# Optimization experiments

Hardware: AMD Instinct MI355X
Metric: run time of the kernel (lower is better)

## Reference

```python
import jax, jax.numpy as jnp
import numpy as np

N = 50000        # nodes
E = 1250000      # edges
B = 512          # graphs
DIN, DH, DOUT = 64, 64, 16


def setup_inputs() -> dict:
    key = jax.random.key(0)
    ks = jax.random.split(key, 8)
    s = lambda d: np.float32(1.0 / np.sqrt(d))
    return {
        "x": jax.random.normal(ks[0], (N, DIN), jnp.float32),
        "edge_index": jax.random.randint(ks[1], (2, E), 0, N, dtype=jnp.int32),
        "batch": jnp.sort(jax.random.randint(ks[2], (N,), 0, B, dtype=jnp.int32)),
        "W1": jax.random.normal(ks[3], (DH, DIN), jnp.float32) * s(DIN),
        "b1": jnp.zeros((DH,), jnp.float32),
        "W2": jax.random.normal(ks[4], (DH, DH), jnp.float32) * s(DH),
        "b2": jnp.zeros((DH,), jnp.float32),
        "W3": jax.random.normal(ks[5], (DH, DH), jnp.float32) * s(DH),
        "b3": jnp.zeros((DH,), jnp.float32),
        "Wl": jax.random.normal(ks[6], (DOUT, DH), jnp.float32) * s(DH),
        "bl": jnp.zeros((DOUT,), jnp.float32),
    }


def _gcn_conv(x, src, dst, norm, W, b, n):
    # PyG GCNConv: h = x W^T; out[i] = sum_{(j->i)} norm_ji * h[j] + b
    h = x @ W.T                                   # [N, DH]
    msg = h[src] * norm[:, None]                  # [E+N, DH] gather
    return jax.ops.segment_sum(msg, dst, num_segments=n) + b


def reference(x, edge_index, batch, W1, b1, W2, b2, W3, b3, Wl, bl):
    n = x.shape[0]
    loop = jnp.arange(n, dtype=edge_index.dtype)
    # add self-loops (PyG GCNConv default add_self_loops=True)
    src = jnp.concatenate([edge_index[0], loop])
    dst = jnp.concatenate([edge_index[1], loop])
    # symmetric normalization: deg^{-1/2}[src] * deg^{-1/2}[dst]
    deg = jax.ops.segment_sum(jnp.ones_like(src, jnp.float32), dst, num_segments=n)
    dinv = jax.lax.rsqrt(deg)                     # deg >= 1 thanks to self-loops
    norm = dinv[src] * dinv[dst]

    h = x
    for W, b in ((W1, b1), (W2, b2), (W3, b3)):
        h = jax.nn.relu(_gcn_conv(h, src, dst, norm, W, b, n))

    # global mean pool over each graph
    sums = jax.ops.segment_sum(h, batch, num_segments=B)          # [B, DH]
    cnts = jax.ops.segment_sum(jnp.ones((n,), jnp.float32), batch, num_segments=B)
    pooled = sums / jnp.maximum(cnts, 1.0)[:, None]
    # dropout p=0.5 is identity in eval mode
    return pooled @ Wl.T + bl                                     # [B, DOUT]
```

## Files before the change

kernel.cpp:

```cpp
#include <hip/hip_runtime.h>
#include <hip/hip_fp16.h>


#define CAPB 3072
#define BINTILE 4096

__global__ __launch_bounds__(256) void init_kernel(int* __restrict__ fctr) {
    int idx = blockIdx.x * blockDim.x + threadIdx.x;
    if (idx < 512) fctr[idx] = 0;
}

__global__ __launch_bounds__(256) void bin512_kernel(const int* __restrict__ src,
                                                     const int* __restrict__ dst,
                                                     int* __restrict__ fctr,
                                                     int2* __restrict__ recs2,
                                                     int e, int n) {
    __shared__ int lcnt[512], gbase[512];
    int tid = threadIdx.x;
    int s0  = blockIdx.x * BINTILE;
    lcnt[tid] = 0;
    lcnt[tid + 256] = 0;
    __syncthreads();
    int dv[16], bk[16];
#pragma unroll
    for (int k = 0; k < 16; ++k) {
        int i = s0 + tid + k * 256;
        if (i < e) {
            dv[k] = dst[i];
            bk[k] = (int)((512LL * dv[k]) / n);
            atomicAdd(&lcnt[bk[k]], 1);
        } else {
            bk[k] = -1;
        }
    }
    __syncthreads();
#pragma unroll
    for (int j = 0; j < 2; ++j) {
        int b = tid + j * 256;
        gbase[b] = b * CAPB + atomicAdd(&fctr[b], lcnt[b]);
        lcnt[b]  = 0;
    }
    __syncthreads();
#pragma unroll
    for (int k = 0; k < 16; ++k) {
        if (bk[k] >= 0) {
            int i = s0 + tid + k * 256;
            int p = gbase[bk[k]] + atomicAdd(&lcnt[bk[k]], 1);
            if (p < (bk[k] + 1) * CAPB) recs2[p] = make_int2(src[i], dv[k]);
        }
    }
}

__global__ __launch_bounds__(256) void sortfill_mm_kernel(
    const int2* __restrict__ recs2, const int* __restrict__ fctr,
    int* __restrict__ rp, float* __restrict__ dinv, int* __restrict__ csr,
    const float* __restrict__ x, const float* __restrict__ W1,
    __half* __restrict__ t1, int n) {
    __shared__ int hist[128];
    __shared__ int lofs[129];
    __shared__ int stage[CAPB];
    __shared__ int redbuf[256];
    __shared__ float xrow[98 * 64];
    int g   = blockIdx.x;
    int N0  = (int)(((long long)n * g + 511) / 512);
    int N1  = (int)(((long long)n * (g + 1) + 511) / 512);
    int nn  = N1 - N0;
    int tid = threadIdx.x;
    int lane = tid & 63;
    int wave = tid >> 6;

    int partial = 0;
    for (int j = tid; j < g; j += 256) partial += min(fctr[j], CAPB);
    redbuf[tid] = partial;
    if (tid < 128) hist[tid] = 0;
    __syncthreads();
    for (int s = 128; s > 0; s >>= 1) {
        if (tid < s) redbuf[tid] += redbuf[tid + s];
        __syncthreads();
    }
    int base = redbuf[0];
    const int2* my = recs2 + (size_t)g * CAPB;
    int total = min(fctr[g], CAPB);
    for (int i = tid; i < total; i += 256)
        atomicAdd(&hist[my[i].y - N0], 1);
    __syncthreads();
    if (tid == 0) {
        int acc = 0;
        for (int k = 0; k < nn; ++k) { lofs[k] = acc; acc += hist[k]; }
        lofs[nn] = acc;
    }
    __syncthreads();
    if (tid < 128) hist[tid] = 0;
    __syncthreads();
    for (int i = tid; i < total; i += 256) {
        int2 rec = my[i];
        int  li  = rec.y - N0;
        int  pos = lofs[li] + atomicAdd(&hist[li], 1);
        stage[pos] = rec.x;
    }
    __syncthreads();
    for (int j = tid; j < total; j += 256) csr[base + j] = stage[j];
    if (tid < nn) {
        rp[N0 + tid]   = base + lofs[tid];
        int deg        = lofs[tid + 1] - lofs[tid];
        dinv[N0 + tid] = rsqrtf((float)(deg + 1));
    }
    if (g == 511 && tid == 0) rp[n] = base + total;

    for (int idx = tid; idx < nn * 16; idx += 256)
        ((float4*)xrow)[idx] = ((const float4*)(x + (size_t)N0 * 64))[idx];
    float4 wreg[16];
    const float4* W4 = (const float4*)(W1 + lane * 64);
#pragma unroll
    for (int q = 0; q < 16; ++q) wreg[q] = W4[q];
    __syncthreads();
    for (int li = wave; li < nn; li += 4) {
        float dv = rsqrtf((float)(lofs[li + 1] - lofs[li] + 1));
        const float4* row = (const float4*)(xrow + li * 64);
        float acc = 0.0f;
#pragma unroll
        for (int q = 0; q < 16; ++q) {
            float4 hv = row[q];
            acc += hv.x * wreg[q].x + hv.y * wreg[q].y +
                   hv.z * wreg[q].z + hv.w * wreg[q].w;
        }
        t1[(size_t)(N0 + li) * 64 + lane] = __float2half(acc * dv);
    }
}

__global__ __launch_bounds__(256) void mm_kernel(const float* __restrict__ h,
                                                 const float* __restrict__ W,
                                                 const float* __restrict__ dinv,
                                                 __half* __restrict__ t, int n) {
    __shared__ float hs[64 * 64];
    int tid  = threadIdx.x;
    int lane = tid & 63;
    int wave = tid >> 6;
    int base = blockIdx.x * 64;

    float4 wreg[16];
    const float4* W4 = (const float4*)(W + lane * 64);
#pragma unroll
    for (int q = 0; q < 16; ++q) wreg[q] = W4[q];

    int nrows = min(64, n - base);
    const float4* h4  = (const float4*)(h + (size_t)base * 64);
    float4*       hs4 = (float4*)hs;
    for (int idx = tid; idx < nrows * 16; idx += 256) hs4[idx] = h4[idx];
    __syncthreads();

    for (int r = wave * 16; r < wave * 16 + 16; ++r) {
        int i = base + r;
        if (i >= n) break;
        const float4* row = (const float4*)(hs + r * 64);
        float acc = 0.0f;
#pragma unroll
        for (int q = 0; q < 16; ++q) {
            float4 hv = row[q];
            acc += hv.x * wreg[q].x + hv.y * wreg[q].y +
                   hv.z * wreg[q].z + hv.w * wreg[q].w;
        }
        t[(size_t)i * 64 + lane] = __float2half(acc * dinv[i]);
    }
}

__global__ __launch_bounds__(256) void agg_kernel(const __half* __restrict__ t,
                                                  const int* __restrict__ rp,
                                                  const int* __restrict__ cs,
                                                  const float* __restrict__ dinv,
                                                  const float* __restrict__ bias,
                                                  float* __restrict__ hout, int n) {
    int gw   = (blockIdx.x * blockDim.x + threadIdx.x) >> 6;
    int lane = threadIdx.x & 63;
    if (gw >= n) return;
    int i   = gw;
    int grp = lane >> 4;
    int fo  = (lane & 15) << 2;
    int beg = rp[i];
    int end = rp[i + 1];

    float4 a0 = make_float4(0.f, 0.f, 0.f, 0.f);
    float4 a1 = a0, a2 = a0, a3 = a0;
    int e = beg + grp;
    for (; e + 12 < end; e += 16) {
        int s0 = cs[e];
        int s1 = cs[e + 4];
        int s2 = cs[e + 8];
        int s3 = cs[e + 12];
        uint2 u0 = *(const uint2*)(t + (size_t)s0 * 64 + fo);
        uint2 u1 = *(const uint2*)(t + (size_t)s1 * 64 + fo);
        uint2 u2 = *(const uint2*)(t + (size_t)s2 * 64 + fo);
        uint2 u3 = *(const uint2*)(t + (size_t)s3 * 64 + fo);
        float2 f;
        f = __half22float2(*(const __half2*)&u0.x); a0.x += f.x; a0.y += f.y;
        f = __half22float2(*(const __half2*)&u0.y); a0.z += f.x; a0.w += f.y;
        f = __half22float2(*(const __half2*)&u1.x); a1.x += f.x; a1.y += f.y;
        f = __half22float2(*(const __half2*)&u1.y); a1.z += f.x; a1.w += f.y;
        f = __half22float2(*(const __half2*)&u2.x); a2.x += f.x; a2.y += f.y;
        f = __half22float2(*(const __half2*)&u2.y); a2.z += f.x; a2.w += f.y;
        f = __half22float2(*(const __half2*)&u3.x); a3.x += f.x; a3.y += f.y;
        f = __half22float2(*(const __half2*)&u3.y); a3.z += f.x; a3.w += f.y;
    }
    for (; e < end; e += 4) {
        int s = cs[e];
        uint2 u = *(const uint2*)(t + (size_t)s * 64 + fo);
        float2 f;
        f = __half22float2(*(const __half2*)&u.x); a1.x += f.x; a1.y += f.y;
        f = __half22float2(*(const __half2*)&u.y); a1.z += f.x; a1.w += f.y;
    }
    float4 acc;
    acc.x = (a0.x + a1.x) + (a2.x + a3.x);
    acc.y = (a0.y + a1.y) + (a2.y + a3.y);
    acc.z = (a0.z + a1.z) + (a2.z + a3.z);
    acc.w = (a0.w + a1.w) + (a2.w + a3.w);
    acc.x += __shfl_xor(acc.x, 16, 64);
    acc.y += __shfl_xor(acc.y, 16, 64);
    acc.z += __shfl_xor(acc.z, 16, 64);
    acc.w += __shfl_xor(acc.w, 16, 64);
    acc.x += __shfl_xor(acc.x, 32, 64);
    acc.y += __shfl_xor(acc.y, 32, 64);
    acc.z += __shfl_xor(acc.z, 32, 64);
    acc.w += __shfl_xor(acc.w, 32, 64);
    if (grp == 0) {
        uint2 su = *(const uint2*)(t + (size_t)i * 64 + fo);
        float2 s01 = __half22float2(*(const __half2*)&su.x);
        float2 s23 = __half22float2(*(const __half2*)&su.y);
        float4 bv = *(const float4*)(bias + fo);
        float  dv = dinv[i];
        float4 o;
        o.x = fmaxf(fmaf(dv, acc.x + s01.x, bv.x), 0.0f);
        o.y = fmaxf(fmaf(dv, acc.y + s01.y, bv.y), 0.0f);
        o.z = fmaxf(fmaf(dv, acc.z + s23.x, bv.z), 0.0f);
        o.w = fmaxf(fmaf(dv, acc.w + s23.y, bv.w), 0.0f);
        *(float4*)(hout + (size_t)i * 64 + fo) = o;
    }
}

__global__ __launch_bounds__(256) void poolfinal_kernel(const float* __restrict__ h,
                                                        const int* __restrict__ batch,
                                                        const float* __restrict__ Wl,
                                                        const float* __restrict__ bl,
                                                        float* __restrict__ out,
                                                        int n) {
    __shared__ float red[4][64];
    int b    = blockIdx.x;
    int tid  = threadIdx.x;
    int lane = tid & 63;
    int w    = tid >> 6;
    int l = 0, r = n;
    while (l < r) { int m = (l + r) >> 1; if (batch[m] < b) l = m + 1; else r = m; }
    int lo = l;
    r = n;
    while (l < r) { int m = (l + r) >> 1; if (batch[m] < b + 1) l = m + 1; else r = m; }
    int hi = l;
    float acc = 0.0f;
    for (int i = lo + w; i < hi; i += 4) acc += h[(size_t)i * 64 + lane];
    red[w][lane] = acc;
    __syncthreads();
    if (w == 0) {
        float s = (red[0][lane] + red[1][lane]) + (red[2][lane] + red[3][lane]);
        float c = (float)(hi - lo);
        red[0][lane] = s / fmaxf(c, 1.0f);
    }
    __syncthreads();
    if (tid < 16) {
        float a = bl[tid];
        const float* wr = Wl + tid * 64;
#pragma unroll
        for (int k = 0; k < 64; ++k) a += red[0][k] * wr[k];
        out[b * 16 + tid] = a;
    }
}

extern "C" void kernel_launch(void* const* d_in, const int* in_sizes, int n_in,
                              void* d_out, int out_size, void* d_ws, size_t ws_size,
                              hipStream_t stream) {
    const float* x    = (const float*)d_in[0];
    const int*   ei   = (const int*)d_in[1];
    const int*   batch= (const int*)d_in[2];
    const float* W1   = (const float*)d_in[3];
    const float* b1   = (const float*)d_in[4];
    const float* W2   = (const float*)d_in[5];
    const float* b2   = (const float*)d_in[6];
    const float* W3   = (const float*)d_in[7];
    const float* b3   = (const float*)d_in[8];
    const float* Wl   = (const float*)d_in[9];
    const float* bl   = (const float*)d_in[10];
    float* out = (float*)d_out;

    int n  = in_sizes[0] / 64;
    int e  = in_sizes[1] / 2;
    int nb = out_size / 16;

    const int* esrc = ei;
    const int* edst = ei + e;

    char* p = (char*)d_ws;
    auto carve = [&](size_t bytes) {
        char* r = p;
        p += (bytes + 255) & ~(size_t)255;
        return r;
    };
    size_t featBytes = (size_t)n * 64 * 4;
    size_t recsBytes = (size_t)512 * CAPB * 8;
    size_t bufBBytes = recsBytes > featBytes ? recsBytes : featBytes;

    float*  dinv = (float*)carve((size_t)n * 4);
    int*    rp   = (int*)  carve((size_t)(n + 1) * 4);
    int*    csr  = (int*)  carve((size_t)e * 4);
    __half* bufT = (__half*)carve((size_t)n * 64 * 2);
    float*  bufB = (float*)carve(bufBBytes);
    int*    fctr = (int*)  carve(512 * 4);
    int2*   recs2 = (int2*)bufB;

    dim3 blk(256);
    int gBIN = (e + BINTILE - 1) / BINTILE;
    int gMM  = (n + 63) / 64;
    int gAGG = (n + 3) / 4;

    init_kernel<<<2, blk, 0, stream>>>(fctr);
    bin512_kernel<<<gBIN, blk, 0, stream>>>(esrc, edst, fctr, recs2, e, n);
    sortfill_mm_kernel<<<512, blk, 0, stream>>>(recs2, fctr, rp, dinv, csr,
                                                x, W1, bufT, n);
    agg_kernel<<<gAGG, blk, 0, stream>>>(bufT, rp, csr, dinv, b1, bufB, n);
    mm_kernel<<<gMM, blk, 0, stream>>>(bufB, W2, dinv, bufT, n);
    agg_kernel<<<gAGG, blk, 0, stream>>>(bufT, rp, csr, dinv, b2, bufB, n);
    mm_kernel<<<gMM, blk, 0, stream>>>(bufB, W3, dinv, bufT, n);
    agg_kernel<<<gAGG, blk, 0, stream>>>(bufT, rp, csr, dinv, b3, bufB, n);
    poolfinal_kernel<<<nb, blk, 0, stream>>>(bufB, batch, Wl, bl, out, n);
}
```

Measured before the change: 308.8 us.

## Fuse GCN aggregation with next-layer matmul and final pooling/linear

Each aggregation kernel now also applies the following layer's weight matrix directly in registers using readlane broadcasts, writing fp16 features for the next layer. This removes the separate mm kernels and the fp32 intermediate feature round trip. The last aggregation projects each node through Wl and atomically adds the count-scaled result into the output, replacing the pooling kernel. Per-graph inverse counts and bias initialisation move into the init kernel. The cost is more per-wave ALU and readlane work, contended atomics on 512x16 outputs, and a float summation order that varies between runs.

```diff
diff --git a/kernel.cpp b/kernel.cpp
--- a/kernel.cpp
+++ b/kernel.cpp
@@ -5,9 +5,28 @@
 #define CAPB 3072
 #define BINTILE 4096
 
-__global__ __launch_bounds__(256) void init_kernel(int* __restrict__ fctr) {
-    int idx = blockIdx.x * blockDim.x + threadIdx.x;
-    if (idx < 512) fctr[idx] = 0;
+__device__ __forceinline__ float rl_f(float v, int l) {
+    return __int_as_float(__builtin_amdgcn_readlane(__float_as_int(v), l));
+}
+
+__global__ __launch_bounds__(256) void init_kernel(int* __restrict__ fctr,
+                                                   const int* __restrict__ batch,
+                                                   const float* __restrict__ bl,
+                                                   float* __restrict__ invc,
+                                                   float* __restrict__ out,
+                                                   int n, int nb) {
+    int t = blockIdx.x * blockDim.x + threadIdx.x;
+    if (t < 512) fctr[t] = 0;
+    if (t < nb) {
+        int l = 0, r = n;
+        while (l < r) { int m = (l + r) >> 1; if (batch[m] < t) l = m + 1; else r = m; }
+        int lo = l;
+        r = n;
+        while (l < r) { int m = (l + r) >> 1; if (batch[m] < t + 1) l = m + 1; else r = m; }
+        invc[t] = 1.0f / fmaxf((float)(l - lo), 1.0f);
+#pragma unroll
+        for (int o = 0; o < 16; ++o) out[t * 16 + o] = bl[o];
+    }
 }
 
 __global__ __launch_bounds__(256) void bin512_kernel(const int* __restrict__ src,
@@ -128,48 +147,13 @@
     }
 }
 
-__global__ __launch_bounds__(256) void mm_kernel(const float* __restrict__ h,
-                                                 const float* __restrict__ W,
-                                                 const float* __restrict__ dinv,
-                                                 __half* __restrict__ t, int n) {
-    __shared__ float hs[64 * 64];
-    int tid  = threadIdx.x;
-    int lane = tid & 63;
-    int wave = tid >> 6;
-    int base = blockIdx.x * 64;
-
-    float4 wreg[16];
-    const float4* W4 = (const float4*)(W + lane * 64);
-#pragma unroll
-    for (int q = 0; q < 16; ++q) wreg[q] = W4[q];
-
-    int nrows = min(64, n - base);
-    const float4* h4  = (const float4*)(h + (size_t)base * 64);
-    float4*       hs4 = (float4*)hs;
-    for (int idx = tid; idx < nrows * 16; idx += 256) hs4[idx] = h4[idx];
-    __syncthreads();
-
-    for (int r = wave * 16; r < wave * 16 + 16; ++r) {
-        int i = base + r;
-        if (i >= n) break;
-        const float4* row = (const float4*)(hs + r * 64);
-        float acc = 0.0f;
-#pragma unroll
-        for (int q = 0; q < 16; ++q) {
-            float4 hv = row[q];
-            acc += hv.x * wreg[q].x + hv.y * wreg[q].y +
-                   hv.z * wreg[q].z + hv.w * wreg[q].w;
-        }
-        t[(size_t)i * 64 + lane] = __float2half(acc * dinv[i]);
-    }
-}
-
-__global__ __launch_bounds__(256) void agg_kernel(const __half* __restrict__ t,
-                                                  const int* __restrict__ rp,
-                                                  const int* __restrict__ cs,
-                                                  const float* __restrict__ dinv,
-                                                  const float* __restrict__ bias,
-                                                  float* __restrict__ hout, int n) {
+__global__ __launch_bounds__(256) void aggmm_kernel(const __half* __restrict__ t,
+                                                    const int* __restrict__ rp,
+                                                    const int* __restrict__ cs,
+                                                    const float* __restrict__ dinv,
+                                                    const float* __restrict__ bias,
+                                                    const float* __restrict__ W,
+                                                    __half* __restrict__ tout, int n) {
     int gw   = (blockIdx.x * blockDim.x + threadIdx.x) >> 6;
     int lane = threadIdx.x & 63;
     if (gw >= n) return;
@@ -221,54 +205,143 @@
     acc.y += __shfl_xor(acc.y, 32, 64);
     acc.z += __shfl_xor(acc.z, 32, 64);
     acc.w += __shfl_xor(acc.w, 32, 64);
-    if (grp == 0) {
-        uint2 su = *(const uint2*)(t + (size_t)i * 64 + fo);
-        float2 s01 = __half22float2(*(const __half2*)&su.x);
-        float2 s23 = __half22float2(*(const __half2*)&su.y);
-        float4 bv = *(const float4*)(bias + fo);
-        float  dv = dinv[i];
-        float4 o;
-        o.x = fmaxf(fmaf(dv, acc.x + s01.x, bv.x), 0.0f);
-        o.y = fmaxf(fmaf(dv, acc.y + s01.y, bv.y), 0.0f);
-        o.z = fmaxf(fmaf(dv, acc.z + s23.x, bv.z), 0.0f);
-        o.w = fmaxf(fmaf(dv, acc.w + s23.y, bv.w), 0.0f);
-        *(float4*)(hout + (size_t)i * 64 + fo) = o;
-    }
-}
-
-__global__ __launch_bounds__(256) void poolfinal_kernel(const float* __restrict__ h,
-                                                        const int* __restrict__ batch,
-                                                        const float* __restrict__ Wl,
-                                                        const float* __restrict__ bl,
-                                                        float* __restrict__ out,
-                                                        int n) {
-    __shared__ float red[4][64];
-    int b    = blockIdx.x;
-    int tid  = threadIdx.x;
-    int lane = tid & 63;
-    int w    = tid >> 6;
-    int l = 0, r = n;
-    while (l < r) { int m = (l + r) >> 1; if (batch[m] < b) l = m + 1; else r = m; }
-    int lo = l;
-    r = n;
-    while (l < r) { int m = (l + r) >> 1; if (batch[m] < b + 1) l = m + 1; else r = m; }
-    int hi = l;
-    float acc = 0.0f;
-    for (int i = lo + w; i < hi; i += 4) acc += h[(size_t)i * 64 + lane];
-    red[w][lane] = acc;
-    __syncthreads();
-    if (w == 0) {
-        float s = (red[0][lane] + red[1][lane]) + (red[2][lane] + red[3][lane]);
-        float c = (float)(hi - lo);
-        red[0][lane] = s / fmaxf(c, 1.0f);
-    }
-    __syncthreads();
-    if (tid < 16) {
-        float a = bl[tid];
-        const float* wr = Wl + tid * 64;
-#pragma unroll
-        for (int k = 0; k < 64; ++k) a += red[0][k] * wr[k];
-        out[b * 16 + tid] = a;
+
+    uint2 su = *(const uint2*)(t + (size_t)i * 64 + fo);
+    float2 s01 = __half22float2(*(const __half2*)&su.x);
+    float2 s23 = __half22float2(*(const __half2*)&su.y);
+    float4 bv = *(const float4*)(bias + fo);
+    float  dv = dinv[i];
+    float4 h4;
+    h4.x = fmaxf(fmaf(dv, acc.x + s01.x, bv.x), 0.0f);
+    h4.y = fmaxf(fmaf(dv, acc.y + s01.y, bv.y), 0.0f);
+    h4.z = fmaxf(fmaf(dv, acc.z + s23.x, bv.z), 0.0f);
+    h4.w = fmaxf(fmaf(dv, acc.w + s23.y, bv.w), 0.0f);
+
+    const float4* W4 = (const float4*)(W + lane * 64);
+    float om = 0.0f;
+    __builtin_amdgcn_sched_barrier(0);
+    {
+        float4 wreg[8];
+#pragma unroll
+        for (int q = 0; q < 8; ++q) wreg[q] = W4[q];
+#pragma unroll
+        for (int c = 0; c < 8; ++c) {
+            om = fmaf(rl_f(h4.x, c), wreg[c].x, om);
+            om = fmaf(rl_f(h4.y, c), wreg[c].y, om);
+            om = fmaf(rl_f(h4.z, c), wreg[c].z, om);
+            om = fmaf(rl_f(h4.w, c), wreg[c].w, om);
+        }
+    }
+    __builtin_amdgcn_sched_barrier(0);
+    {
+        float4 wreg[8];
+#pragma unroll
+        for (int q = 0; q < 8; ++q) wreg[q] = W4[8 + q];
+#pragma unroll
+        for (int c = 0; c < 8; ++c) {
+            om = fmaf(rl_f(h4.x, c + 8), wreg[c].x, om);
+            om = fmaf(rl_f(h4.y, c + 8), wreg[c].y, om);
+            om = fmaf(rl_f(h4.z, c + 8), wreg[c].z, om);
+            om = fmaf(rl_f(h4.w, c + 8), wreg[c].w, om);
+        }
+    }
+    tout[(size_t)i * 64 + lane] = __float2half(om * dv);
+}
+
+__global__ __launch_bounds__(256) void aggfinal_kernel(const __half* __restrict__ t,
+                                                       const int* __restrict__ rp,
+                                                       const int* __restrict__ cs,
+                                                       const float* __restrict__ dinv,
+                                                       const float* __restrict__ bias,
+                                                       const float* __restrict__ Wl,
+                                                       const int* __restrict__ batch,
+                                                       const float* __restrict__ invc,
+                                                       float* __restrict__ out, int n) {
+    int gw   = (blockIdx.x * blockDim.x + threadIdx.x) >> 6;
+    int lane = threadIdx.x & 63;
+    if (gw >= n) return;
+    int i   = gw;
+    int grp = lane >> 4;
+    int fo  = (lane & 15) << 2;
+    int beg = rp[i];
+    int end = rp[i + 1];
+
+    float4 a0 = make_float4(0.f, 0.f, 0.f, 0.f);
+    float4 a1 = a0, a2 = a0, a3 = a0;
+    int e = beg + grp;
+    for (; e + 12 < end; e += 16) {
+        int s0 = cs[e];
+        int s1 = cs[e + 4];
+        int s2 = cs[e + 8];
+        int s3 = cs[e + 12];
+        uint2 u0 = *(const uint2*)(t + (size_t)s0 * 64 + fo);
+        uint2 u1 = *(const uint2*)(t + (size_t)s1 * 64 + fo);
+        uint2 u2 = *(const uint2*)(t + (size_t)s2 * 64 + fo);
+        uint2 u3 = *(const uint2*)(t + (size_t)s3 * 64 + fo);
+        float2 f;
+        f = __half22float2(*(const __half2*)&u0.x); a0.x += f.x; a0.y += f.y;
+        f = __half22float2(*(const __half2*)&u0.y); a0.z += f.x; a0.w += f.y;
+        f = __half22float2(*(const __half2*)&u1.x); a1.x += f.x; a1.y += f.y;
+        f = __half22float2(*(const __half2*)&u1.y); a1.z += f.x; a1.w += f.y;
+        f = __half22float2(*(const __half2*)&u2.x); a2.x += f.x; a2.y += f.y;
+        f = __half22float2(*(const __half2*)&u2.y); a2.z += f.x; a2.w += f.y;
+        f = __half22float2(*(const __half2*)&u3.x); a3.x += f.x; a3.y += f.y;
+        f = __half22float2(*(const __half2*)&u3.y); a3.z += f.x; a3.w += f.y;
+    }
+    for (; e < end; e += 4) {
+        int s = cs[e];
+        uint2 u = *(const uint2*)(t + (size_t)s * 64 + fo);
+        float2 f;
+        f = __half22float2(*(const __half2*)&u.x); a1.x += f.x; a1.y += f.y;
+        f = __half22float2(*(const __half2*)&u.y); a1.z += f.x; a1.w += f.y;
+    }
+    float4 acc;
+    acc.x = (a0.x + a1.x) + (a2.x + a3.x);
+    acc.y = (a0.y + a1.y) + (a2.y + a3.y);
+    acc.z = (a0.z + a1.z) + (a2.z + a3.z);
+    acc.w = (a0.w + a1.w) + (a2.w + a3.w);
+    acc.x += __shfl_xor(acc.x, 16, 64);
+    acc.y += __shfl_xor(acc.y, 16, 64);
+    acc.z += __shfl_xor(acc.z, 16, 64);
+    acc.w += __shfl_xor(acc.w, 16, 64);
+    acc.x += __shfl_xor(acc.x, 32, 64);
+    acc.y += __shfl_xor(acc.y, 32, 64);
+    acc.z += __shfl_xor(acc.z, 32, 64);
+    acc.w += __shfl_xor(acc.w, 32, 64);
+
+    uint2 su = *(const uint2*)(t + (size_t)i * 64 + fo);
+    float2 s01 = __half22float2(*(const __half2*)&su.x);
+    float2 s23 = __half22float2(*(const __half2*)&su.y);
+    float4 bv = *(const float4*)(bias + fo);
+    float  dv = dinv[i];
+    float4 h4;
+    h4.x = fmaxf(fmaf(dv, acc.x + s01.x, bv.x), 0.0f);
+    h4.y = fmaxf(fmaf(dv, acc.y + s01.y, bv.y), 0.0f);
+    h4.z = fmaxf(fmaf(dv, acc.z + s23.x, bv.z), 0.0f);
+    h4.w = fmaxf(fmaf(dv, acc.w + s23.y, bv.w), 0.0f);
+
+    __builtin_amdgcn_sched_barrier(0);
+    float4 wl0 = *(const float4*)(Wl + (0 * 4 + grp) * 64 + fo);
+    float4 wl1 = *(const float4*)(Wl + (1 * 4 + grp) * 64 + fo);
+    float4 wl2 = *(const float4*)(Wl + (2 * 4 + grp) * 64 + fo);
+    float4 wl3 = *(const float4*)(Wl + (3 * 4 + grp) * 64 + fo);
+    float z0 = h4.x * wl0.x + h4.y * wl0.y + h4.z * wl0.z + h4.w * wl0.w;
+    float z1 = h4.x * wl1.x + h4.y * wl1.y + h4.z * wl1.z + h4.w * wl1.w;
+    float z2 = h4.x * wl2.x + h4.y * wl2.y + h4.z * wl2.z + h4.w * wl2.w;
+    float z3 = h4.x * wl3.x + h4.y * wl3.y + h4.z * wl3.z + h4.w * wl3.w;
+#pragma unroll
+    for (int s = 1; s <= 8; s <<= 1) {
+        z0 += __shfl_xor(z0, s, 64);
+        z1 += __shfl_xor(z1, s, 64);
+        z2 += __shfl_xor(z2, s, 64);
+        z3 += __shfl_xor(z3, s, 64);
+    }
+    int m = lane & 15;
+    if (m < 4) {
+        int   b  = batch[i];
+        float ic = invc[b];
+        float zv = (m == 0) ? z0 : (m == 1) ? z1 : (m == 2) ? z2 : z3;
+        atomicAdd(out + b * 16 + (m * 4 + grp), zv * ic);
     }
 }
 
@@ -301,31 +374,25 @@
         p += (bytes + 255) & ~(size_t)255;
         return r;
     };
-    size_t featBytes = (size_t)n * 64 * 4;
-    size_t recsBytes = (size_t)512 * CAPB * 8;
-    size_t bufBBytes = recsBytes > featBytes ? recsBytes : featBytes;
-
-    float*  dinv = (float*)carve((size_t)n * 4);
-    int*    rp   = (int*)  carve((size_t)(n + 1) * 4);
-    int*    csr  = (int*)  carve((size_t)e * 4);
-    __half* bufT = (__half*)carve((size_t)n * 64 * 2);
-    float*  bufB = (float*)carve(bufBBytes);
-    int*    fctr = (int*)  carve(512 * 4);
-    int2*   recs2 = (int2*)bufB;
+    float*  dinv  = (float*)carve((size_t)n * 4);
+    int*    rp    = (int*)  carve((size_t)(n + 1) * 4);
+    int*    csr   = (int*)  carve((size_t)e * 4);
+    __half* tA    = (__half*)carve((size_t)n * 64 * 2);
+    __half* tB    = (__half*)carve((size_t)n * 64 * 2);
+    int2*   recs2 = (int2*) carve((size_t)512 * CAPB * 8);
+    int*    fctr  = (int*)  carve(512 * 4);
+    float*  invc  = (float*)carve((size_t)nb * 4);
 
     dim3 blk(256);
     int gBIN = (e + BINTILE - 1) / BINTILE;
-    int gMM  = (n + 63) / 64;
     int gAGG = (n + 3) / 4;
 
-    init_kernel<<<2, blk, 0, stream>>>(fctr);
+    init_kernel<<<2, blk, 0, stream>>>(fctr, batch, bl, invc, out, n, nb);
     bin512_kernel<<<gBIN, blk, 0, stream>>>(esrc, edst, fctr, recs2, e, n);
     sortfill_mm_kernel<<<512, blk, 0, stream>>>(recs2, fctr, rp, dinv, csr,
-                                                x, W1, bufT, n);
-    agg_kernel<<<gAGG, blk, 0, stream>>>(bufT, rp, csr, dinv, b1, bufB, n);
-    mm_kernel<<<gMM, blk, 0, stream>>>(bufB, W2, dinv, bufT, n);
-    agg_kernel<<<gAGG, blk, 0, stream>>>(bufT, rp, csr, dinv, b2, bufB, n);
-    mm_kernel<<<gMM, blk, 0, stream>>>(bufB, W3, dinv, bufT, n);
-    agg_kernel<<<gAGG, blk, 0, stream>>>(bufT, rp, csr, dinv, b3, bufB, n);
-    poolfinal_kernel<<<nb, blk, 0, stream>>>(bufB, batch, Wl, bl, out, n);
-}
+                                                x, W1, tA, n);
+    aggmm_kernel<<<gAGG, blk, 0, stream>>>(tA, rp, csr, dinv, b1, W2, tB, n);
+    aggmm_kernel<<<gAGG, blk, 0, stream>>>(tB, rp, csr, dinv, b2, W3, tA, n);
+    aggfinal_kernel<<<gAGG, blk, 0, stream>>>(tA, rp, csr, dinv, b3, Wl,
+                                              batch, invc, out, n);
+}
```

Result: slower. 400.7 us (+29.8%).

## Fuse final aggregation with mean-pool and linear head via atomics; rebalance edge loops

Applied to the files above, without the earlier changes.

The last aggregation kernel now applies the output linear layer per node, scales by a precomputed inverse graph size, and atomically adds into the output. This removes the final hidden-feature write and the separate pooling kernel. The init kernel precomputes per-graph inverse counts and seeds the output with the bias. The aggregation loop now splits each node's edges into four contiguous chunks, processes them with a masked, 8-way unrolled loop, and adds an occupancy hint to launch bounds. The trade-off is about 200k float atomics into only 8k output slots, which will contend heavily, and a change in summation order.

```diff
diff --git a/kernel.cpp b/kernel.cpp
--- a/kernel.cpp
+++ b/kernel.cpp
@@ -5,9 +5,24 @@
 #define CAPB 3072
 #define BINTILE 4096
 
-__global__ __launch_bounds__(256) void init_kernel(int* __restrict__ fctr) {
-    int idx = blockIdx.x * blockDim.x + threadIdx.x;
-    if (idx < 512) fctr[idx] = 0;
+__global__ __launch_bounds__(256) void init_kernel(int* __restrict__ fctr,
+                                                   const int* __restrict__ batch,
+                                                   const float* __restrict__ bl,
+                                                   float* __restrict__ invc,
+                                                   float* __restrict__ out,
+                                                   int n, int nb) {
+    int t = blockIdx.x * blockDim.x + threadIdx.x;
+    if (t < 512) fctr[t] = 0;
+    if (t < nb) {
+        int l = 0, r = n;
+        while (l < r) { int m = (l + r) >> 1; if (batch[m] < t) l = m + 1; else r = m; }
+        int lo = l;
+        r = n;
+        while (l < r) { int m = (l + r) >> 1; if (batch[m] < t + 1) l = m + 1; else r = m; }
+        invc[t] = 1.0f / fmaxf((float)(l - lo), 1.0f);
+#pragma unroll
+        for (int o = 0; o < 16; ++o) out[t * 16 + o] = bl[o];
+    }
 }
 
 __global__ __launch_bounds__(256) void bin512_kernel(const int* __restrict__ src,
@@ -164,12 +179,12 @@
     }
 }
 
-__global__ __launch_bounds__(256) void agg_kernel(const __half* __restrict__ t,
-                                                  const int* __restrict__ rp,
-                                                  const int* __restrict__ cs,
-                                                  const float* __restrict__ dinv,
-                                                  const float* __restrict__ bias,
-                                                  float* __restrict__ hout, int n) {
+__global__ __launch_bounds__(256, 6) void agg_kernel(const __half* __restrict__ t,
+                                                     const int* __restrict__ rp,
+                                                     const int* __restrict__ cs,
+                                                     const float* __restrict__ dinv,
+                                                     const float* __restrict__ bias,
+                                                     float* __restrict__ hout, int n) {
     int gw   = (blockIdx.x * blockDim.x + threadIdx.x) >> 6;
     int lane = threadIdx.x & 63;
     if (gw >= n) return;
@@ -178,41 +193,39 @@
     int fo  = (lane & 15) << 2;
     int beg = rp[i];
     int end = rp[i + 1];
-
-    float4 a0 = make_float4(0.f, 0.f, 0.f, 0.f);
-    float4 a1 = a0, a2 = a0, a3 = a0;
-    int e = beg + grp;
-    for (; e + 12 < end; e += 16) {
-        int s0 = cs[e];
-        int s1 = cs[e + 4];
-        int s2 = cs[e + 8];
-        int s3 = cs[e + 12];
-        uint2 u0 = *(const uint2*)(t + (size_t)s0 * 64 + fo);
-        uint2 u1 = *(const uint2*)(t + (size_t)s1 * 64 + fo);
-        uint2 u2 = *(const uint2*)(t + (size_t)s2 * 64 + fo);
-        uint2 u3 = *(const uint2*)(t + (size_t)s3 * 64 + fo);
-        float2 f;
-        f = __half22float2(*(const __half2*)&u0.x); a0.x += f.x; a0.y += f.y;
-        f = __half22float2(*(const __half2*)&u0.y); a0.z += f.x; a0.w += f.y;
-        f = __half22float2(*(const __half2*)&u1.x); a1.x += f.x; a1.y += f.y;
-        f = __half22float2(*(const __half2*)&u1.y); a1.z += f.x; a1.w += f.y;
-        f = __half22float2(*(const __half2*)&u2.x); a2.x += f.x; a2.y += f.y;
-        f = __half22float2(*(const __half2*)&u2.y); a2.z += f.x; a2.w += f.y;
-        f = __half22float2(*(const __half2*)&u3.x); a3.x += f.x; a3.y += f.y;
-        f = __half22float2(*(const __half2*)&u3.y); a3.z += f.x; a3.w += f.y;
-    }
-    for (; e < end; e += 4) {
-        int s = cs[e];
-        uint2 u = *(const uint2*)(t + (size_t)s * 64 + fo);
-        float2 f;
-        f = __half22float2(*(const __half2*)&u.x); a1.x += f.x; a1.y += f.y;
-        f = __half22float2(*(const __half2*)&u.y); a1.z += f.x; a1.w += f.y;
+    uint2 su = *(const uint2*)(t + (size_t)i * 64 + fo);
+    float dv = dinv[i];
+    float4 bv = *(const float4*)(bias + fo);
+
+    int deg = end - beg;
+    int len = (deg + 3) >> 2;
+    int gb  = beg + grp * len;
+    int ge  = min(gb + len, end);
+
+    float4 aa[4];
+    aa[0] = make_float4(0.f, 0.f, 0.f, 0.f);
+    aa[1] = aa[0]; aa[2] = aa[0]; aa[3] = aa[0];
+    for (int eb = gb; eb < ge; eb += 8) {
+#pragma unroll
+        for (int j = 0; j < 8; ++j) {
+            int   ej = eb + j;
+            int   ec = min(ej, end - 1);
+            int   sj = cs[ec];
+            uint2 u  = *(const uint2*)(t + (size_t)sj * 64 + fo);
+            float m  = (ej < ge) ? 1.0f : 0.0f;
+            float2 f0 = __half22float2(*(const __half2*)&u.x);
+            float2 f1 = __half22float2(*(const __half2*)&u.y);
+            aa[j & 3].x = fmaf(m, f0.x, aa[j & 3].x);
+            aa[j & 3].y = fmaf(m, f0.y, aa[j & 3].y);
+            aa[j & 3].z = fmaf(m, f1.x, aa[j & 3].z);
+            aa[j & 3].w = fmaf(m, f1.y, aa[j & 3].w);
+        }
     }
     float4 acc;
-    acc.x = (a0.x + a1.x) + (a2.x + a3.x);
-    acc.y = (a0.y + a1.y) + (a2.y + a3.y);
-    acc.z = (a0.z + a1.z) + (a2.z + a3.z);
-    acc.w = (a0.w + a1.w) + (a2.w + a3.w);
+    acc.x = (aa[0].x + aa[1].x) + (aa[2].x + aa[3].x);
+    acc.y = (aa[0].y + aa[1].y) + (aa[2].y + aa[3].y);
+    acc.z = (aa[0].z + aa[1].z) + (aa[2].z + aa[3].z);
+    acc.w = (aa[0].w + aa[1].w) + (aa[2].w + aa[3].w);
     acc.x += __shfl_xor(acc.x, 16, 64);
     acc.y += __shfl_xor(acc.y, 16, 64);
     acc.z += __shfl_xor(acc.z, 16, 64);
@@ -222,11 +235,8 @@
     acc.z += __shfl_xor(acc.z, 32, 64);
     acc.w += __shfl_xor(acc.w, 32, 64);
     if (grp == 0) {
-        uint2 su = *(const uint2*)(t + (size_t)i * 64 + fo);
         float2 s01 = __half22float2(*(const __half2*)&su.x);
         float2 s23 = __half22float2(*(const __half2*)&su.y);
-        float4 bv = *(const float4*)(bias + fo);
-        float  dv = dinv[i];
         float4 o;
         o.x = fmaxf(fmaf(dv, acc.x + s01.x, bv.x), 0.0f);
         o.y = fmaxf(fmaf(dv, acc.y + s01.y, bv.y), 0.0f);
@@ -236,39 +246,94 @@
     }
 }
 
-__global__ __launch_bounds__(256) void poolfinal_kernel(const float* __restrict__ h,
-                                                        const int* __restrict__ batch,
-                                                        const float* __restrict__ Wl,
-                                                        const float* __restrict__ bl,
-                                                        float* __restrict__ out,
-                                                        int n) {
-    __shared__ float red[4][64];
-    int b    = blockIdx.x;
-    int tid  = threadIdx.x;
-    int lane = tid & 63;
-    int w    = tid >> 6;
-    int l = 0, r = n;
-    while (l < r) { int m = (l + r) >> 1; if (batch[m] < b) l = m + 1; else r = m; }
-    int lo = l;
-    r = n;
-    while (l < r) { int m = (l + r) >> 1; if (batch[m] < b + 1) l = m + 1; else r = m; }
-    int hi = l;
-    float acc = 0.0f;
-    for (int i = lo + w; i < hi; i += 4) acc += h[(size_t)i * 64 + lane];
-    red[w][lane] = acc;
-    __syncthreads();
-    if (w == 0) {
-        float s = (red[0][lane] + red[1][lane]) + (red[2][lane] + red[3][lane]);
-        float c = (float)(hi - lo);
-        red[0][lane] = s / fmaxf(c, 1.0f);
-    }
-    __syncthreads();
-    if (tid < 16) {
-        float a = bl[tid];
-        const float* wr = Wl + tid * 64;
-#pragma unroll
-        for (int k = 0; k < 64; ++k) a += red[0][k] * wr[k];
-        out[b * 16 + tid] = a;
+__global__ __launch_bounds__(256, 6) void aggfinal_kernel(const __half* __restrict__ t,
+                                                          const int* __restrict__ rp,
+                                                          const int* __restrict__ cs,
+                                                          const float* __restrict__ dinv,
+                                                          const float* __restrict__ bias,
+                                                          const float* __restrict__ Wl,
+                                                          const int* __restrict__ batch,
+                                                          const float* __restrict__ invc,
+                                                          float* __restrict__ out, int n) {
+    int gw   = (blockIdx.x * blockDim.x + threadIdx.x) >> 6;
+    int lane = threadIdx.x & 63;
+    if (gw >= n) return;
+    int i   = gw;
+    int grp = lane >> 4;
+    int fo  = (lane & 15) << 2;
+    int beg = rp[i];
+    int end = rp[i + 1];
+    uint2 su = *(const uint2*)(t + (size_t)i * 64 + fo);
+    float dv = dinv[i];
+    float4 bv = *(const float4*)(bias + fo);
+
+    int deg = end - beg;
+    int len = (deg + 3) >> 2;
+    int gb  = beg + grp * len;
+    int ge  = min(gb + len, end);
+
+    float4 aa[4];
+    aa[0] = make_float4(0.f, 0.f, 0.f, 0.f);
+    aa[1] = aa[0]; aa[2] = aa[0]; aa[3] = aa[0];
+    for (int eb = gb; eb < ge; eb += 8) {
+#pragma unroll
+        for (int j = 0; j < 8; ++j) {
+            int   ej = eb + j;
+            int   ec = min(ej, end - 1);
+            int   sj = cs[ec];
+            uint2 u  = *(const uint2*)(t + (size_t)sj * 64 + fo);
+            float m  = (ej < ge) ? 1.0f : 0.0f;
+            float2 f0 = __half22float2(*(const __half2*)&u.x);
+            float2 f1 = __half22float2(*(const __half2*)&u.y);
+            aa[j & 3].x = fmaf(m, f0.x, aa[j & 3].x);
+            aa[j & 3].y = fmaf(m, f0.y, aa[j & 3].y);
+            aa[j & 3].z = fmaf(m, f1.x, aa[j & 3].z);
+            aa[j & 3].w = fmaf(m, f1.y, aa[j & 3].w);
+        }
+    }
+    float4 acc;
+    acc.x = (aa[0].x + aa[1].x) + (aa[2].x + aa[3].x);
+    acc.y = (aa[0].y + aa[1].y) + (aa[2].y + aa[3].y);
+    acc.z = (aa[0].z + aa[1].z) + (aa[2].z + aa[3].z);
+    acc.w = (aa[0].w + aa[1].w) + (aa[2].w + aa[3].w);
+    acc.x += __shfl_xor(acc.x, 16, 64);
+    acc.y += __shfl_xor(acc.y, 16, 64);
+    acc.z += __shfl_xor(acc.z, 16, 64);
+    acc.w += __shfl_xor(acc.w, 16, 64);
+    acc.x += __shfl_xor(acc.x, 32, 64);
+    acc.y += __shfl_xor(acc.y, 32, 64);
+    acc.z += __shfl_xor(acc.z, 32, 64);
+    acc.w += __shfl_xor(acc.w, 32, 64);
+
+    float2 s01 = __half22float2(*(const __half2*)&su.x);
+    float2 s23 = __half22float2(*(const __half2*)&su.y);
+    float4 h4;
+    h4.x = fmaxf(fmaf(dv, acc.x + s01.x, bv.x), 0.0f);
+    h4.y = fmaxf(fmaf(dv, acc.y + s01.y, bv.y), 0.0f);
+    h4.z = fmaxf(fmaf(dv, acc.z + s23.x, bv.z), 0.0f);
+    h4.w = fmaxf(fmaf(dv, acc.w + s23.y, bv.w), 0.0f);
+
+    float4 wl0 = *(const float4*)(Wl + (0 * 4 + grp) * 64 + fo);
+    float4 wl1 = *(const float4*)(Wl + (1 * 4 + grp) * 64 + fo);
+    float4 wl2 = *(const float4*)(Wl + (2 * 4 + grp) * 64 + fo);
+    float4 wl3 = *(const float4*)(Wl + (3 * 4 + grp) * 64 + fo);
+    float z0 = h4.x * wl0.x + h4.y * wl0.y + h4.z * wl0.z + h4.w * wl0.w;
+    float z1 = h4.x * wl1.x + h4.y * wl1.y + h4.z * wl1.z + h4.w * wl1.w;
+    float z2 = h4.x * wl2.x + h4.y * wl2.y + h4.z * wl2.z + h4.w * wl2.w;
+    float z3 = h4.x * wl3.x + h4.y * wl3.y + h4.z * wl3.z + h4.w * wl3.w;
+#pragma unroll
+    for (int s = 1; s <= 8; s <<= 1) {
+        z0 += __shfl_xor(z0, s, 64);
+        z1 += __shfl_xor(z1, s, 64);
+        z2 += __shfl_xor(z2, s, 64);
+        z3 += __shfl_xor(z3, s, 64);
+    }
+    int m = lane & 15;
+    if (m < 4) {
+        int   b  = batch[i];
+        float ic = invc[b];
+        float zv = (m == 0) ? z0 : (m == 1) ? z1 : (m == 2) ? z2 : z3;
+        atomicAdd(out + b * 16 + (m * 4 + grp), zv * ic);
     }
 }
 
@@ -311,6 +376,7 @@
     __half* bufT = (__half*)carve((size_t)n * 64 * 2);
     float*  bufB = (float*)carve(bufBBytes);
     int*    fctr = (int*)  carve(512 * 4);
+    float*  invc = (float*)carve((size_t)nb * 4);
     int2*   recs2 = (int2*)bufB;
 
     dim3 blk(256);
@@ -318,7 +384,7 @@
     int gMM  = (n + 63) / 64;
     int gAGG = (n + 3) / 4;
 
-    init_kernel<<<2, blk, 0, stream>>>(fctr);
+    init_kernel<<<2, blk, 0, stream>>>(fctr, batch, bl, invc, out, n, nb);
     bin512_kernel<<<gBIN, blk, 0, stream>>>(esrc, edst, fctr, recs2, e, n);
     sortfill_mm_kernel<<<512, blk, 0, stream>>>(recs2, fctr, rp, dinv, csr,
                                                 x, W1, bufT, n);
@@ -326,6 +392,6 @@
     mm_kernel<<<gMM, blk, 0, stream>>>(bufB, W2, dinv, bufT, n);
     agg_kernel<<<gAGG, blk, 0, stream>>>(bufT, rp, csr, dinv, b2, bufB, n);
     mm_kernel<<<gMM, blk, 0, stream>>>(bufB, W3, dinv, bufT, n);
-    agg_kernel<<<gAGG, blk, 0, stream>>>(bufT, rp, csr, dinv, b3, bufB, n);
-    poolfinal_kernel<<<nb, blk, 0, stream>>>(bufB, batch, Wl, bl, out, n);
-}
+    aggfinal_kernel<<<gAGG, blk, 0, stream>>>(bufT, rp, csr, dinv, b3, Wl,
+                                              batch, invc, out, n);
+}
```

Measured after the change: 288.2 us. 6.7% less time.
